# Optimization experiments

Hardware: AMD Instinct MI355X
Metric: run time of the kernel (lower is better)

## Reference

```python
import jax, jax.numpy as jnp
import numpy as np
import math

B, S, D, H = 1, 2048, 4096, 32
HD = D // H  # 128
BASE = 10000.0
NEG = -1e9


def rotate_half(x):
    x1, x2 = x[..., : x.shape[-1] // 2], x[..., x.shape[-1] // 2 :]
    return jnp.concatenate((-x2, x1), axis=-1)


def setup_inputs() -> dict:
    key = jax.random.key(0)
    ks = jax.random.split(key, 5)
    scale = 1.0 / math.sqrt(D)
    hidden_states = jax.random.normal(ks[0], (B, S, D), dtype=jnp.float32)
    Wq = jax.random.normal(ks[1], (D, D), dtype=jnp.float32) * scale
    Wk = jax.random.normal(ks[2], (D, D), dtype=jnp.float32) * scale
    Wv = jax.random.normal(ks[3], (D, D), dtype=jnp.float32) * scale
    Wo = jax.random.normal(ks[4], (D, D), dtype=jnp.float32) * scale
    # causal additive mask [1,1,S,S]
    causal = jnp.tril(jnp.ones((S, S), dtype=bool))
    attention_mask = jnp.where(causal, 0.0, NEG).astype(jnp.float32)[None, None]
    # rotary cos/sin cache [1,1,S,HD]
    inv_freq = 1.0 / (BASE ** (jnp.arange(0, HD, 2, dtype=jnp.float32) / HD))
    freqs = jnp.arange(S, dtype=jnp.float32)[:, None] * inv_freq[None, :]
    emb = jnp.concatenate((freqs, freqs), axis=-1)
    cos = jnp.cos(emb)[None, None]
    sin = jnp.sin(emb)[None, None]
    return dict(hidden_states=hidden_states, attention_mask=attention_mask,
                cos=cos, sin=sin, Wq=Wq, Wk=Wk, Wv=Wv, Wo=Wo)


def reference(hidden_states, attention_mask, cos, sin, Wq, Wk, Wv, Wo):
    b, s, d = hidden_states.shape
    # projections (torch Linear: x @ W.T), reshape to [B,H,S,HD]
    def proj(W):
        return (hidden_states @ W.T).reshape(b, s, H, HD).transpose(0, 2, 1, 3)
    q, k, v = proj(Wq), proj(Wk), proj(Wv)
    # RoPE
    q = q * cos + rotate_half(q) * sin
    k = k * cos + rotate_half(k) * sin
    # scores [B,H,S,S], key pre-scaled as in original
    scores = jnp.einsum('bhqd,bhkd->bhqk', q, k / math.sqrt(HD)) + attention_mask
    attn = jax.nn.softmax(scores.astype(jnp.float32), axis=-1).astype(scores.dtype)
    out = jnp.einsum('bhqk,bhkd->bhqd', attn, v)
    out = out.transpose(0, 2, 1, 3).reshape(b, s, d)
    return out @ Wo.T
```

## Files before the change

### kernel.cpp

```cpp
#include <hip/hip_runtime.h>
#include <hip/hip_bf16.h>
#include <stdint.h>

#define DEV __device__ __forceinline__

typedef __bf16 bf16x8 __attribute__((ext_vector_type(8)));
typedef float f32x4 __attribute__((ext_vector_type(4)));
typedef unsigned short ushort8_t __attribute__((ext_vector_type(8)));
typedef unsigned short ushort4_t __attribute__((ext_vector_type(4)));

constexpr int S = 2048;
constexpr int D = 4096;
constexpr int H = 32;
constexpr int HD = 128;
constexpr float kSc = 0.08838834764831845f * 1.4426950408889634f;

DEV unsigned short f2bf(float f) {
    uint32_t u = __builtin_bit_cast(uint32_t, f);
    u += 0x7fffu + ((u >> 16) & 1u);
    return (unsigned short)(u >> 16);
}
DEV float bf2f(unsigned short h) {
    uint32_t u = ((uint32_t)h) << 16;
    return __builtin_bit_cast(float, u);
}

DEV void gload_lds16(const void* g, void* l) {
    __builtin_amdgcn_global_load_lds(
        (const __attribute__((address_space(1))) void*)g,
        (__attribute__((address_space(3))) void*)l,
        16, 0, 0);
}

DEV f32x4 mfma16(bf16x8 a, bf16x8 b, f32x4 c) {
    return __builtin_amdgcn_mfma_f32_16x16x32_bf16(a, b, c, 0, 0, 0);
}

__global__ __launch_bounds__(256) void cvt_all(const float* __restrict__ hs,
                                               const float* __restrict__ w0,
                                               const float* __restrict__ w1,
                                               const float* __restrict__ w2,
                                               const float* __restrict__ w3,
                                               unsigned short* __restrict__ hsb,
                                               unsigned short* __restrict__ o0,
                                               unsigned short* __restrict__ o1,
                                               unsigned short* __restrict__ o2,
                                               unsigned short* __restrict__ o3) {
    const int b = blockIdx.x;
    const float* in;
    unsigned short* out;
    size_t blk;
    if (b < 4096) {
        in = hs; out = hsb; blk = (size_t)b;
    } else {
        const int i = b - 4096;
        const int w = i >> 13;
        const int r = i & 8191;
        in  = (w == 0) ? w0 : (w == 1) ? w1 : (w == 2) ? w2 : w3;
        out = (w == 0) ? o0 : (w == 1) ? o1 : (w == 2) ? o2 : o3;
        blk = (size_t)r;
    }
    const size_t i8 = blk * 256 + threadIdx.x;
    f32x4 a = ((const f32x4*)in)[2 * i8];
    f32x4 c = ((const f32x4*)in)[2 * i8 + 1];
    ushort8_t o;
    o[0] = f2bf(a[0]); o[1] = f2bf(a[1]); o[2] = f2bf(a[2]); o[3] = f2bf(a[3]);
    o[4] = f2bf(c[0]); o[5] = f2bf(c[1]); o[6] = f2bf(c[2]); o[7] = f2bf(c[3]);
    ((ushort8_t*)out)[i8] = o;
}

template <int BN, int OMODE>
__global__ __launch_bounds__(512, 2) void gemm8(const unsigned short* __restrict__ Ap,
                                                const unsigned short* __restrict__ Bp,
                                                unsigned short* __restrict__ Oq,
                                                unsigned short* __restrict__ Ok,
                                                unsigned short* __restrict__ Ovt,
                                                float* __restrict__ Of) {
    constexpr int NT = BN / 64;
    constexpr int NB = BN / 64;
    extern __shared__ unsigned short lds8[];
    unsigned short (*As)[8192] = (unsigned short(*)[8192])lds8;
    unsigned short* Bs0 = lds8 + 4 * 8192;
    unsigned short* Bs1 = Bs0 + BN * 64;

    const int tix = threadIdx.x;
    const int lane = tix & 63;
    const int w = tix >> 6;
    const int g = lane >> 4;
    const int rl = lane & 15;
    const int wm = w >> 2;
    const int wn = w & 3;
    const int bc0 = wn * (BN / 4);
    const int rx = rl & 7;

    const int yy = blockIdx.x & 7;
    const int xx = blockIdx.x >> 3;
    const int m0 = yy * 256;
    const int n0 = xx * BN;

    int srowA[2], scolA[2];
#pragma unroll
    for (int u = 0; u < 2; ++u) {
        const int c = u * 512 + tix;
        srowA[u] = c >> 3;
        scolA[u] = ((c & 7) ^ (srowA[u] & 7)) << 3;
    }
    int srowB[NB], scolB[NB];
#pragma unroll
    for (int u = 0; u < NB; ++u) {
        const int c = u * 512 + tix;
        srowB[u] = c >> 3;
        scolB[u] = ((c & 7) ^ (srowB[u] & 7)) << 3;
    }

    const char* aBase[2] = {(const char*)As[wm], (const char*)As[2 + wm]};
    const char* bBase[2] = {(const char*)Bs0, (const char*)Bs1};

    f32x4 acc[4][2][NT] = {};
    bf16x8 bfr[NT][2];

#define STG_A8(t, h, slot)                                                        \
    if ((t) < 64) {                                                               \
        _Pragma("unroll") for (int u = 0; u < 2; ++u)                             \
            gload_lds16(Ap + (size_t)(m0 + (h) * 128 + srowA[u]) * 4096 +         \
                            (t) * 64 + scolA[u],                                  \
                        &As[slot][(u * 512 + tix) * 8]);                          \
    }
#define STG_B8(t, slot)                                                           \
    if ((t) < 64) {                                                               \
        unsigned short* bs_ = (slot) ? Bs1 : Bs0;                                 \
        _Pragma("unroll") for (int u = 0; u < NB; ++u)                            \
            gload_lds16(Bp + (size_t)(n0 + srowB[u]) * 4096 +                     \
                            (t) * 64 + scolB[u],                                  \
                        &bs_[(u * 512 + tix) * 8]);                               \
    }

#define PHASE8(pt, q, STG, VM)                                                    \
    {                                                                             \
        bf16x8 af[2][2];                                                          \
        _Pragma("unroll") for (int mi = 0; mi < 2; ++mi)                          \
        _Pragma("unroll") for (int ks = 0; ks < 2; ++ks) {                        \
            const int ab = ((q) * 32 + mi * 16 + rl) * 128 +                      \
                           ((((ks << 2) + g) ^ rx) << 4);                         \
            af[mi][ks] = *(const bf16x8*)(aBase[pt] + ab);                        \
        }                                                                         \
        if ((q) == 0) {                                                           \
            _Pragma("unroll") for (int nt = 0; nt < NT; ++nt)                     \
            _Pragma("unroll") for (int ks = 0; ks < 2; ++ks) {                    \
                const int bb = (bc0 + nt * 16 + rl) * 128 +                       \
                               ((((ks << 2) + g) ^ rx) << 4);                     \
                bfr[nt][ks] = *(const bf16x8*)(bBase[pt] + bb);                   \
            }                                                                     \
        }                                                                         \
        STG;                                                                      \
        if (VM) {                                                                 \
            if (last) {                                                           \
                asm volatile("s_waitcnt vmcnt(0)" ::: "memory");                  \
            } else if constexpr (NB == 3) {                                       \
                asm volatile("s_waitcnt vmcnt(3)" ::: "memory");                  \
            } else {                                                              \
                asm volatile("s_waitcnt vmcnt(2)" ::: "memory");                  \
            }                                                                     \
        }                                                                         \
        __builtin_amdgcn_s_barrier();                                             \
        __builtin_amdgcn_s_setprio(1);                                            \
        _Pragma("unroll") for (int ks = 0; ks < 2; ++ks)                          \
        _Pragma("unroll") for (int mi = 0; mi < 2; ++mi)                          \
        _Pragma("unroll") for (int nt = 0; nt < NT; ++nt)                         \
            acc[q][mi][nt] = mfma16(af[mi][ks], bfr[nt][ks], acc[q][mi][nt]);     \
        __builtin_amdgcn_s_setprio(0);                                            \
        __builtin_amdgcn_s_barrier();                                             \
    }

    STG_A8(0, 0, 0); STG_A8(0, 1, 1);
    STG_B8(0, 0); STG_B8(1, 1);
    __syncthreads();

    for (int i = 0; i < 32; ++i) {
        const bool last = (i == 31);
        const int o = 2 * i + 1, ne = 2 * i + 2, no = 2 * i + 3;
        PHASE8(0, 0, STG_A8(o, 0, 2), 0)
        PHASE8(0, 1, STG_A8(o, 1, 3), 0)
        PHASE8(0, 2, STG_B8(ne, 0), 0)
        PHASE8(0, 3, ((void)0), 1)
        PHASE8(1, 0, STG_A8(ne, 0, 0), 0)
        PHASE8(1, 1, STG_A8(ne, 1, 1), 0)
        PHASE8(1, 2, STG_B8(no, 1), 0)
        PHASE8(1, 3, ((void)0), 1)
    }
#undef PHASE8
#undef STG_A8
#undef STG_B8

#pragma unroll
    for (int q = 0; q < 4; ++q)
#pragma unroll
        for (int mi = 0; mi < 2; ++mi)
#pragma unroll
            for (int nt = 0; nt < NT; ++nt) {
                const int row0 = m0 + wm * 128 + q * 32 + mi * 16 + g * 4;
                const int gc = n0 + bc0 + nt * 16 + rl;
                if constexpr (OMODE == 0) {
                    const int sel = gc >> 12;
                    const int col = gc & 4095;
                    if (sel == 2) {
                        ushort4_t v;
#pragma unroll
                        for (int r = 0; r < 4; ++r) v[r] = f2bf(acc[q][mi][nt][r]);
                        *(ushort4_t*)&Ovt[(size_t)col * S + row0] = v;
                    } else {
                        unsigned short* op = sel ? Ok : Oq;
#pragma unroll
                        for (int r = 0; r < 4; ++r)
                            op[(size_t)(row0 + r) * 4096 + col] = f2bf(acc[q][mi][nt][r]);
                    }
                } else {
#pragma unroll
                    for (int r = 0; r < 4; ++r)
                        Of[(size_t)(row0 + r) * 4096 + gc] = acc[q][mi][nt][r];
                }
            }
}

__global__ __launch_bounds__(256) void rope_kernel(unsigned short* __restrict__ Qb,
                                                   unsigned short* __restrict__ Kb,
                                                   const float* __restrict__ cosT,
                                                   const float* __restrict__ sinT) {
    const int i = blockIdx.x * 256 + threadIdx.x;
    const int j8 = i & 7;
    const int h = (i >> 3) & 31;
    const int s = i >> 8;
    const size_t base = (size_t)s * D + h * HD + j8 * 8;
    const float* cp = cosT + s * HD + j8 * 8;
    const float* sp = sinT + s * HD + j8 * 8;
    float c1[8], s1[8], c2[8], s2[8];
#pragma unroll
    for (int k = 0; k < 8; ++k) { c1[k] = cp[k]; s1[k] = sp[k]; c2[k] = cp[k + 64]; s2[k] = sp[k + 64]; }

#pragma unroll
    for (int w = 0; w < 2; ++w) {
        unsigned short* p = (w == 0 ? Qb : Kb) + base;
        const float f = (w == 0) ? kSc : 1.0f;
        ushort8_t x1 = *(ushort8_t*)p;
        ushort8_t x2 = *(ushort8_t*)(p + 64);
        ushort8_t o1, o2;
#pragma unroll
        for (int k = 0; k < 8; ++k) {
            const float a = bf2f(x1[k]);
            const float b = bf2f(x2[k]);
            o1[k] = f2bf((a * c1[k] - b * s1[k]) * f);
            o2[k] = f2bf((b * c2[k] + a * s2[k]) * f);
        }
        *(ushort8_t*)p = o1;
        *(ushort8_t*)(p + 64) = o2;
    }
}

__global__ __launch_bounds__(512, 2) void flash_attn(const unsigned short* __restrict__ Q,
                                                     const unsigned short* __restrict__ K,
                                                     const unsigned short* __restrict__ V,
                                                     unsigned short* __restrict__ O) {
    extern __shared__ unsigned short ldsA[];

    const int t = threadIdx.x;
    const int lane = t & 63;
    const int wid = t >> 6;
    const int g = lane >> 4;
    const int rl = lane & 15;
    const int bid = blockIdx.x;
    const int p = 7 - (bid >> 5);
    const int h = bid & 31;
    const int qt = (wid < 4) ? (8 + p) : (7 - p);
    const int wrow0 = qt * 128 + (wid & 3) * 32;

    bf16x8 qf[2][4];
#pragma unroll
    for (int mi = 0; mi < 2; ++mi) {
        const unsigned short* qp = Q + (size_t)(wrow0 + mi * 16 + rl) * D + h * HD;
#pragma unroll
        for (int ks = 0; ks < 4; ++ks) qf[mi][ks] = *(const bf16x8*)(qp + ks * 32 + g * 8);
    }

    f32x4 accO[2][8] = {};
    float m2s[2] = {-1e30f, -1e30f};
    float lsum[2] = {0.f, 0.f};

#pragma unroll
    for (int r = 0; r < 2; ++r) {
        const int c = r * 512 + t;
        const int rowk = c >> 4;
        const int srck = (c & 15) ^ (rowk & 7);
        gload_lds16(K + (size_t)rowk * D + h * HD + srck * 8, &ldsA[c * 8]);
    }
    __syncthreads();

    int cur = 0;
    const int ntiles = 2 * (8 + p) + 2;
    for (int kv = 0; kv < ntiles; ++kv) {
        const int kv0 = kv * 64;
#pragma unroll
        for (int r = 0; r < 2; ++r) {
            const int c = r * 512 + t;
            const int rowv = c >> 3;
            const int srcv = (c & 7) ^ (rowv & 7);
            gload_lds16(V + (size_t)(h * HD + rowv) * S + kv0 + srcv * 8,
                        &ldsA[16384 + c * 8]);
        }
        if (kv + 1 < ntiles) {
#pragma unroll
            for (int r = 0; r < 2; ++r) {
                const int c = r * 512 + t;
                const int rowk = c >> 4;
                const int srck = (c & 15) ^ (rowk & 7);
                gload_lds16(K + (size_t)(kv0 + 64 + rowk) * D + h * HD + srck * 8,
                            &ldsA[(cur ^ 1) * 8192 + c * 8]);
            }
        }

        const bool active = kv0 <= wrow0 + 31;
        if (active) {
            const unsigned short* KsC = ldsA + cur * 8192;
            f32x4 sf[2][4];
#pragma unroll
            for (int mi = 0; mi < 2; ++mi)
#pragma unroll
                for (int nt = 0; nt < 4; ++nt) sf[mi][nt] = f32x4{0.f, 0.f, 0.f, 0.f};
            __builtin_amdgcn_s_setprio(1);
#pragma unroll
            for (int nt = 0; nt < 4; ++nt) {
                const int row = nt * 16 + rl;
#pragma unroll
                for (int ks = 0; ks < 4; ++ks) {
                    bf16x8 kf = *(const bf16x8*)&KsC[row * 128 + (((ks * 4 + g) ^ (row & 7)) << 3)];
                    sf[0][nt] = mfma16(kf, qf[0][ks], sf[0][nt]);
                    sf[1][nt] = mfma16(kf, qf[1][ks], sf[1][nt]);
                }
            }
            __builtin_amdgcn_s_setprio(0);

            const bool needMask = (kv0 + 63 > wrow0);
            float cf2[2];
            bool chg = false;
#pragma unroll
            for (int mi = 0; mi < 2; ++mi) {
                const int qrow = wrow0 + mi * 16 + rl;
                float mx = -1e30f;
                if (needMask) {
#pragma unroll
                    for (int nt = 0; nt < 4; ++nt)
#pragma unroll
                        for (int r = 0; r < 4; ++r) {
                            const int kcol = kv0 + nt * 16 + g * 4 + r;
                            float s = sf[mi][nt][r];
                            s = (kcol > qrow) ? -1e30f : s;
                            sf[mi][nt][r] = s;
                            mx = fmaxf(mx, s);
                        }
                } else {
#pragma unroll
                    for (int nt = 0; nt < 4; ++nt)
#pragma unroll
                        for (int r = 0; r < 4; ++r) mx = fmaxf(mx, sf[mi][nt][r]);
                }
                mx = fmaxf(mx, __shfl_xor(mx, 16));
                mx = fmaxf(mx, __shfl_xor(mx, 32));
                const float mn = (mx <= m2s[mi] + 8.f) ? m2s[mi] : mx;
                cf2[mi] = __builtin_amdgcn_exp2f(m2s[mi] - mn);
                chg |= (mn > m2s[mi]);
                m2s[mi] = mn;
                float rs = 0.f;
#pragma unroll
                for (int nt = 0; nt < 4; ++nt)
#pragma unroll
                    for (int r = 0; r < 4; ++r) {
                        const float pv = __builtin_amdgcn_exp2f(sf[mi][nt][r] - mn);
                        sf[mi][nt][r] = pv;
                        rs += pv;
                    }
                rs += __shfl_xor(rs, 16);
                rs += __shfl_xor(rs, 32);
                lsum[mi] = lsum[mi] * cf2[mi] + rs;
            }

            if (__any((int)chg)) {
#pragma unroll
                for (int mi = 0; mi < 2; ++mi)
#pragma unroll
                    for (int nt = 0; nt < 8; ++nt)
#pragma unroll
                        for (int r = 0; r < 4; ++r) accO[mi][nt][r] *= cf2[mi];
            }

            unsigned short* myP = ldsA + 24576 + wid * 2048;
#pragma unroll
            for (int mi = 0; mi < 2; ++mi) {
                const int row = mi * 16 + rl;
                const int rxp = row & 7;
#pragma unroll
                for (int nt = 0; nt < 4; ++nt) {
                    ushort4_t v;
#pragma unroll
                    for (int r = 0; r < 4; ++r) v[r] = f2bf(sf[mi][nt][r]);
                    const int chunk = nt * 2 + (g >> 1);
                    *(ushort4_t*)&myP[row * 64 + ((chunk ^ rxp) << 3) + ((g & 1) << 2)] = v;
                }
            }
        }
        __syncthreads();

        if (active) {
            unsigned short* myP = ldsA + 24576 + wid * 2048;
            const unsigned short* VsC = ldsA + 16384;
            __builtin_amdgcn_s_setprio(1);
#pragma unroll
            for (int ks = 0; ks < 2; ++ks) {
                bf16x8 pa[2];
#pragma unroll
                for (int mi = 0; mi < 2; ++mi) {
                    const int row = mi * 16 + rl;
                    pa[mi] = *(const bf16x8*)&myP[row * 64 + (((ks * 4 + g) ^ (row & 7)) << 3)];
                }
#pragma unroll
                for (int nt = 0; nt < 8; ++nt) {
                    const int vrow = nt * 16 + rl;
                    bf16x8 vf = *(const bf16x8*)&VsC[vrow * 64 + (((ks * 4 + g) ^ (vrow & 7)) << 3)];
                    accO[0][nt] = mfma16(vf, pa[0], accO[0][nt]);
                    accO[1][nt] = mfma16(vf, pa[1], accO[1][nt]);
                }
            }
            __builtin_amdgcn_s_setprio(0);
        }
        __syncthreads();
        cur ^= 1;
    }

#pragma unroll
    for (int mi = 0; mi < 2; ++mi) {
        const float inv = 1.0f / lsum[mi];
        const int qrow = wrow0 + mi * 16 + rl;
#pragma unroll
        for (int nt = 0; nt < 8; ++nt) {
            ushort4_t v;
#pragma unroll
            for (int r = 0; r < 4; ++r) v[r] = f2bf(accO[mi][nt][r] * inv);
            *(ushort4_t*)&O[(size_t)qrow * D + h * HD + nt * 16 + g * 4] = v;
        }
    }
}

extern "C" void kernel_launch(void* const* d_in, const int* in_sizes, int n_in,
                              void* d_out, int out_size, void* d_ws, size_t ws_size,
                              hipStream_t stream) {
    const float* hs   = (const float*)d_in[0];
    const float* cosT = (const float*)d_in[2];
    const float* sinT = (const float*)d_in[3];
    const float* Wq   = (const float*)d_in[4];
    const float* Wk   = (const float*)d_in[5];
    const float* Wv   = (const float*)d_in[6];
    const float* Wo   = (const float*)d_in[7];

    char* ws = (char*)d_ws;
    const size_t MB = 1ull << 20;
    unsigned short* hsb = (unsigned short*)(ws);
    unsigned short* wqb = (unsigned short*)(ws + 16 * MB);
    unsigned short* wkb = (unsigned short*)(ws + 48 * MB);
    unsigned short* wvb = (unsigned short*)(ws + 80 * MB);
    unsigned short* wob = (unsigned short*)(ws + 112 * MB);
    unsigned short* Qb  = (unsigned short*)(ws + 144 * MB);
    unsigned short* Kb  = (unsigned short*)(ws + 160 * MB);
    unsigned short* Vt  = (unsigned short*)(ws + 176 * MB);
    unsigned short* AOb = (unsigned short*)(ws + 192 * MB);

    cvt_all<<<4096 + 4 * 8192, 256, 0, stream>>>(hs, Wq, Wk, Wv, Wo,
                                                 hsb, wqb, wkb, wvb, wob);

    gemm8<192, 0><<<512, 512, 114688, stream>>>(hsb, wqb, Qb, Kb, Vt, nullptr);

    rope_kernel<<<2048, 256, 0, stream>>>(Qb, Kb, cosT, sinT);

    flash_attn<<<256, 512, 81920, stream>>>(Qb, Kb, Vt, AOb);

    gemm8<128, 1><<<256, 512, 98304, stream>>>(AOb, wob, nullptr, nullptr, nullptr,
                                               (float*)d_out);
}
```

Before: 413.3 us.

## Triple-buffer A tiles in QKV GEMM to prefetch two K-steps ahead

Splits the templated GEMM into a dedicated QKV kernel and an output-projection kernel. The QKV kernel now keeps three A-tile buffers and issues loads two K-steps ahead, using a looser vmcnt wait, so more global-to-LDS latency is hidden behind MFMA work. LDS use rises from 112KB to 144KB per block. With launch bounds asking for two blocks per CU, this may reduce occupancy if two blocks no longer fit in LDS.

```diff
diff --git a/kernel.cpp b/kernel.cpp
--- a/kernel.cpp
+++ b/kernel.cpp
@@ -69,15 +69,152 @@
     ((ushort8_t*)out)[i8] = o;
 }
 
-template <int BN, int OMODE>
-__global__ __launch_bounds__(512, 2) void gemm8(const unsigned short* __restrict__ Ap,
-                                                const unsigned short* __restrict__ Bp,
-                                                unsigned short* __restrict__ Oq,
-                                                unsigned short* __restrict__ Ok,
-                                                unsigned short* __restrict__ Ovt,
-                                                float* __restrict__ Of) {
-    constexpr int NT = BN / 64;
-    constexpr int NB = BN / 64;
+__global__ __launch_bounds__(512, 2) void gemm_qkv8d(const unsigned short* __restrict__ Ap,
+                                                     const unsigned short* __restrict__ Bp,
+                                                     unsigned short* __restrict__ Oq,
+                                                     unsigned short* __restrict__ Ok,
+                                                     unsigned short* __restrict__ Ovt) {
+    constexpr int NT = 3;
+    extern __shared__ unsigned short lds8[];
+
+    const int tix = threadIdx.x;
+    const int lane = tix & 63;
+    const int w = tix >> 6;
+    const int g = lane >> 4;
+    const int rl = lane & 15;
+    const int wm = w >> 2;
+    const int wn = w & 3;
+    const int bc0 = wn * 48;
+    const int rx = rl & 7;
+
+    const int yy = blockIdx.x & 7;
+    const int xx = blockIdx.x >> 3;
+    const int m0 = yy * 256;
+    const int n0 = xx * 192;
+
+    int srowA[2], scolA[2];
+#pragma unroll
+    for (int u = 0; u < 2; ++u) {
+        const int c = u * 512 + tix;
+        srowA[u] = c >> 3;
+        scolA[u] = ((c & 7) ^ (srowA[u] & 7)) << 3;
+    }
+    int srowB[3], scolB[3];
+#pragma unroll
+    for (int u = 0; u < 3; ++u) {
+        const int c = u * 512 + tix;
+        srowB[u] = c >> 3;
+        scolB[u] = ((c & 7) ^ (srowB[u] & 7)) << 3;
+    }
+
+    f32x4 acc[4][2][NT] = {};
+    bf16x8 bfr[NT][2];
+
+#define STG_A(t, h)                                                               \
+    if ((t) < 64) {                                                               \
+        unsigned short* as_ = lds8 + (((t) % 3) * 2 + (h)) * 8192;                \
+        _Pragma("unroll") for (int u = 0; u < 2; ++u)                             \
+            gload_lds16(Ap + (size_t)(m0 + (h) * 128 + srowA[u]) * 4096 +         \
+                            (t) * 64 + scolA[u],                                  \
+                        &as_[(u * 512 + tix) * 8]);                               \
+    }
+#define STG_B(t)                                                                  \
+    if ((t) < 64) {                                                               \
+        unsigned short* bs_ = lds8 + 49152 + ((t) & 1) * 12288;                   \
+        _Pragma("unroll") for (int u = 0; u < 3; ++u)                             \
+            gload_lds16(Bp + (size_t)(n0 + srowB[u]) * 4096 +                     \
+                            (t) * 64 + scolB[u],                                  \
+                        &bs_[(u * 512 + tix) * 8]);                               \
+    }
+
+#define PH(pp, bb, q, STG, VM)                                                    \
+    {                                                                             \
+        const char* aB = (const char*)(lds8 + ((pp) * 2 + wm) * 8192);            \
+        const char* bB = (const char*)(lds8 + 49152 + (bb) * 12288);              \
+        bf16x8 af[2][2];                                                          \
+        _Pragma("unroll") for (int mi = 0; mi < 2; ++mi)                          \
+        _Pragma("unroll") for (int ks = 0; ks < 2; ++ks) {                        \
+            const int ab = ((q) * 32 + mi * 16 + rl) * 128 +                      \
+                           ((((ks << 2) + g) ^ rx) << 4);                         \
+            af[mi][ks] = *(const bf16x8*)(aB + ab);                               \
+        }                                                                         \
+        if ((q) == 0) {                                                           \
+            _Pragma("unroll") for (int nt = 0; nt < NT; ++nt)                     \
+            _Pragma("unroll") for (int ks = 0; ks < 2; ++ks) {                    \
+                const int bb2 = (bc0 + nt * 16 + rl) * 128 +                      \
+                                ((((ks << 2) + g) ^ rx) << 4);                    \
+                bfr[nt][ks] = *(const bf16x8*)(bB + bb2);                         \
+            }                                                                     \
+        }                                                                         \
+        STG;                                                                      \
+        if (VM) {                                                                 \
+            if (last) {                                                           \
+                asm volatile("s_waitcnt vmcnt(0)" ::: "memory");                  \
+            } else {                                                              \
+                asm volatile("s_waitcnt vmcnt(7)" ::: "memory");                  \
+            }                                                                     \
+        }                                                                         \
+        __builtin_amdgcn_s_barrier();                                             \
+        __builtin_amdgcn_s_setprio(1);                                            \
+        _Pragma("unroll") for (int ks = 0; ks < 2; ++ks)                          \
+        _Pragma("unroll") for (int mi = 0; mi < 2; ++mi)                          \
+        _Pragma("unroll") for (int nt = 0; nt < NT; ++nt)                         \
+            acc[q][mi][nt] = mfma16(af[mi][ks], bfr[nt][ks], acc[q][mi][nt]);     \
+        __builtin_amdgcn_s_setprio(0);                                            \
+        __builtin_amdgcn_s_barrier();                                             \
+    }
+
+    STG_A(0, 0); STG_A(0, 1);
+    STG_A(1, 0); STG_A(1, 1);
+    STG_B(0); STG_B(1);
+    __syncthreads();
+
+    for (int i = 0; i < 32; ++i) {
+        const bool last = (i == 31);
+        const int e = 2 * i, o = 2 * i + 1;
+        const int pe = e % 3;
+        const int po = (e + 1) % 3;
+        PH(pe, 0, 0, STG_A(e + 2, 0), 0)
+        PH(pe, 0, 1, STG_A(e + 2, 1), 0)
+        PH(pe, 0, 2, STG_B(e + 2), 0)
+        PH(pe, 0, 3, ((void)0), 1)
+        PH(po, 1, 0, STG_A(o + 2, 0), 0)
+        PH(po, 1, 1, STG_A(o + 2, 1), 0)
+        PH(po, 1, 2, STG_B(o + 2), 0)
+        PH(po, 1, 3, ((void)0), 1)
+    }
+#undef PH
+#undef STG_A
+#undef STG_B
+
+#pragma unroll
+    for (int q = 0; q < 4; ++q)
+#pragma unroll
+        for (int mi = 0; mi < 2; ++mi)
+#pragma unroll
+            for (int nt = 0; nt < NT; ++nt) {
+                const int row0 = m0 + wm * 128 + q * 32 + mi * 16 + g * 4;
+                const int gc = n0 + bc0 + nt * 16 + rl;
+                const int sel = gc >> 12;
+                const int col = gc & 4095;
+                if (sel == 2) {
+                    ushort4_t v;
+#pragma unroll
+                    for (int r = 0; r < 4; ++r) v[r] = f2bf(acc[q][mi][nt][r]);
+                    *(ushort4_t*)&Ovt[(size_t)col * S + row0] = v;
+                } else {
+                    unsigned short* op = sel ? Ok : Oq;
+#pragma unroll
+                    for (int r = 0; r < 4; ++r)
+                        op[(size_t)(row0 + r) * 4096 + col] = f2bf(acc[q][mi][nt][r]);
+                }
+            }
+}
+
+__global__ __launch_bounds__(512, 2) void gemm_out8(const unsigned short* __restrict__ Ap,
+                                                    const unsigned short* __restrict__ Bp,
+                                                    float* __restrict__ Of) {
+    constexpr int BN = 128, NT = 2, NB = 2;
     extern __shared__ unsigned short lds8[];
     unsigned short (*As)[8192] = (unsigned short(*)[8192])lds8;
     unsigned short* Bs0 = lds8 + 4 * 8192;
@@ -156,8 +293,6 @@
         if (VM) {                                                                 \
             if (last) {                                                           \
                 asm volatile("s_waitcnt vmcnt(0)" ::: "memory");                  \
-            } else if constexpr (NB == 3) {                                       \
-                asm volatile("s_waitcnt vmcnt(3)" ::: "memory");                  \
             } else {                                                              \
                 asm volatile("s_waitcnt vmcnt(2)" ::: "memory");                  \
             }                                                                     \
@@ -200,25 +335,9 @@
             for (int nt = 0; nt < NT; ++nt) {
                 const int row0 = m0 + wm * 128 + q * 32 + mi * 16 + g * 4;
                 const int gc = n0 + bc0 + nt * 16 + rl;
-                if constexpr (OMODE == 0) {
-                    const int sel = gc >> 12;
-                    const int col = gc & 4095;
-                    if (sel == 2) {
-                        ushort4_t v;
-#pragma unroll
-                        for (int r = 0; r < 4; ++r) v[r] = f2bf(acc[q][mi][nt][r]);
-                        *(ushort4_t*)&Ovt[(size_t)col * S + row0] = v;
-                    } else {
-                        unsigned short* op = sel ? Ok : Oq;
-#pragma unroll
-                        for (int r = 0; r < 4; ++r)
-                            op[(size_t)(row0 + r) * 4096 + col] = f2bf(acc[q][mi][nt][r]);
-                    }
-                } else {
-#pragma unroll
-                    for (int r = 0; r < 4; ++r)
-                        Of[(size_t)(row0 + r) * 4096 + gc] = acc[q][mi][nt][r];
-                }
+#pragma unroll
+                for (int r = 0; r < 4; ++r)
+                    Of[(size_t)(row0 + r) * 4096 + gc] = acc[q][mi][nt][r];
             }
 }
 
@@ -474,12 +593,11 @@
     cvt_all<<<4096 + 4 * 8192, 256, 0, stream>>>(hs, Wq, Wk, Wv, Wo,
                                                  hsb, wqb, wkb, wvb, wob);
 
-    gemm8<192, 0><<<512, 512, 114688, stream>>>(hsb, wqb, Qb, Kb, Vt, nullptr);
+    gemm_qkv8d<<<512, 512, 147456, stream>>>(hsb, wqb, Qb, Kb, Vt);
 
     rope_kernel<<<2048, 256, 0, stream>>>(Qb, Kb, cosT, sinT);
 
     flash_attn<<<256, 512, 81920, stream>>>(Qb, Kb, Vt, AOb);
 
-    gemm8<128, 1><<<256, 512, 98304, stream>>>(AOb, wob, nullptr, nullptr, nullptr,
-                                               (float*)d_out);
-}
+    gemm_out8<<<256, 512, 98304, stream>>>(AOb, wob, (float*)d_out);
+}
```

Measured after the change: 410.7 us (median of 3 runs). About the same (-0.6%).
